# Kernel tuning notes

Hardware: AMD Instinct MI355X
Metric: run time of the kernel (lower is better)

The kernel has to match this reference:

```python
import jax, jax.numpy as jnp
import numpy as np

N_NODES = 100000
N_EDGES = 1600000  # directed, src < dst; to_undirected doubles them
N_GRAPHS = 128
D_IN, D_H, D_FC, N_CLS = 128, 64, 32, 10


def setup_inputs() -> dict:
    key = jax.random.key(0)
    ks = jax.random.split(key, 12)
    x = jax.random.normal(ks[0], (N_NODES, D_IN), dtype=jnp.float32)
    # edges with src < dst so concatenating the flipped copy yields the undirected set
    r = jax.random.randint(ks[1], (2, N_EDGES), 0, N_NODES, dtype=jnp.int64)
    src = jnp.minimum(r[0], r[1])
    dst = jnp.maximum(r[0], r[1])
    dst = jnp.where(src == dst, (dst + 1) % N_NODES, dst)  # avoid pre-existing self loops
    edge_index = jnp.stack([src, dst])
    batch = jnp.sort(jax.random.randint(ks[2], (N_NODES,), 0, N_GRAPHS, dtype=jnp.int64))
    sc = lambda f: 1.0 / jnp.sqrt(jnp.float32(f))
    return {
        "x": x,
        "edge_index": edge_index,
        "batch": batch,
        "W_in": jax.random.normal(ks[3], (D_IN, D_H), jnp.float32) * sc(D_IN),
        "b_in": jnp.zeros((D_H,), jnp.float32),
        "W1": jax.random.normal(ks[4], (D_H, D_H), jnp.float32) * sc(D_H),
        "b1": jnp.zeros((D_H,), jnp.float32),
        "W2": jax.random.normal(ks[5], (D_H, D_H), jnp.float32) * sc(D_H),
        "b2": jnp.zeros((D_H,), jnp.float32),
        "Wf1": jax.random.normal(ks[6], (D_H, D_FC), jnp.float32) * sc(D_H),
        "bf1": jnp.zeros((D_FC,), jnp.float32),
        "Wf2": jax.random.normal(ks[7], (D_FC, N_CLS), jnp.float32) * sc(D_FC),
        "bf2": jnp.zeros((N_CLS,), jnp.float32),
    }


def _gcn_conv(x, W, b, src, dst, dinv, n_nodes):
    # GCNConv: x' = D^{-1/2}(A+I)D^{-1/2} (xW) + b, dinv = deg^{-1/2} incl. self loops
    xw = x @ W
    norm = (dinv[src] * dinv[dst])[:, None]              # [E,1]
    agg = jax.ops.segment_sum(xw[src] * norm, dst, num_segments=n_nodes)
    agg = agg + xw * (dinv * dinv)[:, None]              # self-loop term
    return agg + b


def reference(x, edge_index, batch, W_in, b_in, W1, b1, W2, b2, Wf1, bf1, Wf2, bf2):
    n = x.shape[0]
    # to_undirected: append reversed edges (inputs have src<dst, so no dup dirs)
    src = jnp.concatenate([edge_index[0], edge_index[1]])
    dst = jnp.concatenate([edge_index[1], edge_index[0]])
    # degree including self loop
    deg = 1.0 + jax.ops.segment_sum(jnp.ones_like(dst, dtype=x.dtype), dst, num_segments=n)
    dinv = jax.lax.rsqrt(deg)

    h = jax.nn.relu(x @ W_in + b_in)
    h = jax.nn.relu(_gcn_conv(h, W1, b1, src, dst, dinv, n))
    h = jax.nn.relu(_gcn_conv(h, W2, b2, src, dst, dinv, n))

    # global_mean_pool over graph ids
    sums = jax.ops.segment_sum(h, batch, num_segments=N_GRAPHS)
    cnts = jax.ops.segment_sum(jnp.ones((n,), h.dtype), batch, num_segments=N_GRAPHS)
    pooled = sums / jnp.maximum(cnts, 1.0)[:, None]

    g = jax.nn.relu(pooled @ Wf1 + bf1)
    logits = g @ Wf2 + bf2
    return jax.nn.log_softmax(logits, axis=1)
```

## Files before the change

kernel.cpp:

```cpp
#include <hip/hip_runtime.h>
#include <hip/hip_fp16.h>
#include <math.h>

constexpr int DG  = 128;
constexpr int DIN = 128;
constexpr int DH  = 64;
constexpr int DFC = 32;
constexpr int DC  = 10;
constexpr int CAP    = 80;
constexpr int NB     = 2048;
constexpr int ABLK   = 256;
constexpr int SCAP   = 2048;
constexpr int MAXNPB = 52;

__global__ __launch_bounds__(256) void k_hist(const int* __restrict__ src,
                                              const int* __restrict__ dst,
                                              int* __restrict__ histT,
                                              int E, int EPB, int NPB) {
    __shared__ int h[NB];
    for (int i = threadIdx.x; i < NB; i += 256) h[i] = 0;
    __syncthreads();
    int e0 = blockIdx.x * EPB, e1 = min(e0 + EPB, E);
    for (int i = e0 + threadIdx.x; i < e1; i += 256) {
        int u = src[i], v = dst[i];
        atomicAdd(&h[v / NPB], 1);
        atomicAdd(&h[u / NPB], 1);
    }
    __syncthreads();
    for (int i = threadIdx.x; i < NB; i += 256)
        histT[(size_t)i * ABLK + blockIdx.x] = h[i];
}

__global__ __launch_bounds__(256) void k_expand(const int* __restrict__ histT,
                                                int* __restrict__ baseT,
                                                int* __restrict__ ecnt,
                                                float* __restrict__ sums,
                                                int* __restrict__ cnts) {
    __shared__ int s[256];
    int b = blockIdx.x, t = threadIdx.x;
    int v = histT[(size_t)b * ABLK + t];
    s[t] = v;
    __syncthreads();
    for (int o = 1; o < 256; o <<= 1) {
        int tv = (t >= o) ? s[t - o] : 0;
        __syncthreads();
        s[t] += tv;
        __syncthreads();
    }
    int incl = s[t];
    baseT[(size_t)b * ABLK + t] = b * SCAP + incl - v;
    if (t == 255) ecnt[b] = min(incl, SCAP);
    int gid = b * 256 + t;
    if (gid < DG * DH) sums[gid] = 0.0f;
    if (gid < DG) cnts[gid] = 0;
}

__global__ __launch_bounds__(256) void k_binplace(const int* __restrict__ src,
                                                  const int* __restrict__ dst,
                                                  const int* __restrict__ baseT,
                                                  int* __restrict__ staging,
                                                  int E, int EPB, int NPB) {
    __shared__ int lcnt[NB];
    __shared__ int lbase[NB];
    int blk = blockIdx.x;
    for (int i = threadIdx.x; i < NB; i += 256) {
        lcnt[i]  = 0;
        lbase[i] = baseT[(size_t)i * ABLK + blk];
    }
    __syncthreads();
    int e0 = blk * EPB, e1 = min(e0 + EPB, E);
    for (int i = e0 + threadIdx.x; i < e1; i += 256) {
        int u = src[i], v = dst[i];
        int bv = v / NPB, bu = u / NPB;
        int rv = atomicAdd(&lcnt[bv], 1);
        int sv = lbase[bv] + rv;
        if (sv < (bv + 1) * SCAP) staging[sv] = ((v - bv * NPB) << 17) | u;
        int ru = atomicAdd(&lcnt[bu], 1);
        int su = lbase[bu] + ru;
        if (su < (bu + 1) * SCAP) staging[su] = ((u - bu * NPB) << 17) | v;
    }
}

__global__ __launch_bounds__(256) void k_rows(const int* __restrict__ staging,
                                              const int* __restrict__ ecnt,
                                              int* __restrict__ adj,
                                              int* __restrict__ cnt,
                                              float* __restrict__ dinv,
                                              int N, int NPB) {
    __shared__ int rows[MAXNPB * CAP];
    __shared__ int cur[MAXNPB];
    int b = blockIdx.x;
    int nbase = b * NPB;
    int nn = min(NPB, N - nbase);
    if (nn <= 0) return;
    for (int i = threadIdx.x; i < nn; i += 256) cur[i] = 0;
    __syncthreads();
    int s0 = b * SCAP, s1 = s0 + ecnt[b];
    for (int i = s0 + threadIdx.x; i < s1; i += 256) {
        int e  = staging[i];
        int vl = e >> 17;
        int u  = e & 0x1FFFF;
        int p  = atomicAdd(&cur[vl], 1);
        if (p < CAP) rows[vl * CAP + p] = u;
    }
    __syncthreads();
    for (int s = threadIdx.x; s < nn * CAP; s += 256) {
        int node = s / CAP, p = s - node * CAP;
        if (p < min(cur[node], CAP))
            adj[(size_t)(nbase + node) * CAP + p] = rows[s];
    }
    for (int i = threadIdx.x; i < nn; i += 256) {
        int c = cur[i];
        cnt[nbase + i]  = c;
        dinv[nbase + i] = rsqrtf(1.0f + (float)c);
    }
}

__global__ __launch_bounds__(256) void k_lin_in(const float* __restrict__ x,
                                                const float* __restrict__ W,
                                                const float* __restrict__ b,
                                                __half* __restrict__ out, int n) {
    __shared__ float sx[16 * DIN];
    __shared__ float part[16 * 4 * DH];
    int t = threadIdx.x;
    int lane = t & 63, w = t >> 6;
    float wreg[32];
#pragma unroll
    for (int i = 0; i < 32; i++) wreg[i] = W[(w * 32 + i) * DH + lane];
    float bb = b[lane];
    int tile = blockIdx.x * 16;
    const float4* xsrc = (const float4*)(x + (size_t)tile * DIN);
    float4* sx4 = (float4*)sx;
    sx4[t]       = xsrc[t];
    sx4[t + 256] = xsrc[t + 256];
    __syncthreads();
#pragma unroll 1
    for (int r = 0; r < 16; r++) {
        const float4* xr = (const float4*)(sx + r * DIN + w * 32);
        float a0 = 0.f, a1 = 0.f, a2 = 0.f, a3 = 0.f;
#pragma unroll
        for (int q = 0; q < 8; q++) {
            float4 xv = xr[q];
            a0 = fmaf(xv.x, wreg[q * 4 + 0], a0);
            a1 = fmaf(xv.y, wreg[q * 4 + 1], a1);
            a2 = fmaf(xv.z, wreg[q * 4 + 2], a2);
            a3 = fmaf(xv.w, wreg[q * 4 + 3], a3);
        }
        part[(r * 4 + w) * DH + lane] = (a0 + a1) + (a2 + a3);
    }
    __syncthreads();
#pragma unroll
    for (int q = 0; q < 4; q++) {
        int r = w * 4 + q;
        float s = part[(r * 4 + 0) * DH + lane] + part[(r * 4 + 1) * DH + lane]
                + part[(r * 4 + 2) * DH + lane] + part[(r * 4 + 3) * DH + lane] + bb;
        out[(size_t)(tile + r) * DH + lane] = __float2half(fmaxf(s, 0.0f));
    }
}

__global__ __launch_bounds__(256) void k_mm64(const __half* __restrict__ h,
                                              const float* __restrict__ W,
                                              const float* __restrict__ dinv,
                                              __half* __restrict__ out, int n) {
    __shared__ float sx[16 * DH];
    int t = threadIdx.x, lane = t & 63, w = t >> 6;
    float wreg[64];
#pragma unroll
    for (int i = 0; i < 64; i++) wreg[i] = W[i * DH + lane];
    int tile = blockIdx.x * 16;
    {
        const __half2* hsrc = (const __half2*)(h + (size_t)tile * DH);
        float2* sx2 = (float2*)sx;
        sx2[t * 2]     = __half22float2(hsrc[t * 2]);
        sx2[t * 2 + 1] = __half22float2(hsrc[t * 2 + 1]);
    }
    __syncthreads();
#pragma unroll
    for (int q = 0; q < 4; q++) {
        int r = w * 4 + q;
        const float4* xr = (const float4*)(sx + r * DH);
        float a0 = 0.f, a1 = 0.f, a2 = 0.f, a3 = 0.f;
#pragma unroll
        for (int p = 0; p < 16; p++) {
            float4 xv = xr[p];
            a0 = fmaf(xv.x, wreg[p * 4 + 0], a0);
            a1 = fmaf(xv.y, wreg[p * 4 + 1], a1);
            a2 = fmaf(xv.z, wreg[p * 4 + 2], a2);
            a3 = fmaf(xv.w, wreg[p * 4 + 3], a3);
        }
        float dv = dinv[tile + r];
        out[(size_t)(tile + r) * DH + lane] = __float2half(((a0 + a1) + (a2 + a3)) * dv);
    }
}

__global__ __launch_bounds__(256) void k_gather(const int* __restrict__ cnt,
                                                const int* __restrict__ adj,
                                                const __half2* __restrict__ xws,
                                                const float* __restrict__ dinv,
                                                const float* __restrict__ b,
                                                __half* __restrict__ out, int n) {
    int lane = threadIdx.x & 63;
    int v    = blockIdx.x * 4 + (threadIdx.x >> 6);
    if (v >= n) return;
    int half_id = lane >> 5, fp = lane & 31;
    int len = min(cnt[v], CAP);
    const int* row = adj + (size_t)v * CAP;
    int idx = 0;
    if (lane < len) idx = row[lane];
    int len64 = min(len, 64);
    float ax0 = 0.f, ay0 = 0.f, ax1 = 0.f, ay1 = 0.f;
    float ax2 = 0.f, ay2 = 0.f, ax3 = 0.f, ay3 = 0.f;
    int k = half_id;
    for (; k + 6 < len64; k += 8) {
        int u0 = __shfl(idx, k);
        int u1 = __shfl(idx, k + 2);
        int u2 = __shfl(idx, k + 4);
        int u3 = __shfl(idx, k + 6);
        float2 f0 = __half22float2(xws[(size_t)u0 * 32 + fp]);
        float2 f1 = __half22float2(xws[(size_t)u1 * 32 + fp]);
        float2 f2 = __half22float2(xws[(size_t)u2 * 32 + fp]);
        float2 f3 = __half22float2(xws[(size_t)u3 * 32 + fp]);
        ax0 += f0.x; ay0 += f0.y; ax1 += f1.x; ay1 += f1.y;
        ax2 += f2.x; ay2 += f2.y; ax3 += f3.x; ay3 += f3.y;
    }
    for (; k < len64; k += 2) {
        int u0 = __shfl(idx, k);
        float2 f0 = __half22float2(xws[(size_t)u0 * 32 + fp]);
        ax0 += f0.x; ay0 += f0.y;
    }
    for (int j = 64 + half_id; j < len; j += 2) {
        float2 f0 = __half22float2(xws[(size_t)row[j] * 32 + fp]);
        ax0 += f0.x; ay0 += f0.y;
    }
    float ax = (ax0 + ax1) + (ax2 + ax3);
    float ay = (ay0 + ay1) + (ay2 + ay3);
    ax += __shfl_xor(ax, 32);
    ay += __shfl_xor(ay, 32);
    if (half_id == 0) {
        float2 s  = __half22float2(xws[(size_t)v * 32 + fp]);
        float  dv = dinv[v];
        float2 bb = ((const float2*)b)[fp];
        __half2 o = __floats2half2_rn(fmaxf(dv * (ax + s.x) + bb.x, 0.0f),
                                      fmaxf(dv * (ay + s.y) + bb.y, 0.0f));
        ((__half2*)out)[(size_t)v * 32 + fp] = o;
    }
}

__global__ __launch_bounds__(256) void k_pool(const __half* __restrict__ h,
                                              const int* __restrict__ batch,
                                              float* __restrict__ sums,
                                              int* __restrict__ cnts, int n) {
    int lane = threadIdx.x & 63;
    int w    = blockIdx.x * 4 + (threadIdx.x >> 6);
    int start = w * 64;
    if (start >= n) return;
    int end  = min(start + 64, n);
    int curg = batch[start];
    float acc = 0.f;
    int   c   = 0;
    for (int node = start; node < end; node++) {
        int g = batch[node];
        if (g != curg) {
            atomicAdd(&sums[curg * DH + lane], acc);
            if (lane == 0) atomicAdd(&cnts[curg], c);
            acc = 0.f; c = 0; curg = g;
        }
        acc += __half2float(h[(size_t)node * DH + lane]);
        c++;
    }
    atomicAdd(&sums[curg * DH + lane], acc);
    if (lane == 0) atomicAdd(&cnts[curg], c);
}

__global__ __launch_bounds__(64) void k_head(const float* __restrict__ sums,
                                             const int* __restrict__ cnts,
                                             const float* __restrict__ Wf1,
                                             const float* __restrict__ bf1,
                                             const float* __restrict__ Wf2,
                                             const float* __restrict__ bf2,
                                             float* __restrict__ out) {
    int g = blockIdx.x, lane = threadIdx.x;
    float cnt    = (float)max(cnts[g], 1);
    float pooled = sums[g * DH + lane] / cnt;
    float acc = (lane < DFC) ? bf1[lane] : 0.f;
    for (int k = 0; k < DH; k++) {
        float pk = __shfl(pooled, k);
        if (lane < DFC) acc = fmaf(pk, Wf1[k * DFC + lane], acc);
    }
    float gv = fmaxf(acc, 0.f);
    float acc2 = (lane < DC) ? bf2[lane] : 0.f;
    for (int k = 0; k < DFC; k++) {
        float gk = __shfl(gv, k);
        if (lane < DC) acc2 = fmaf(gk, Wf2[k * DC + lane], acc2);
    }
    float v = (lane < DC) ? acc2 : -INFINITY;
    float m = v;
    for (int o = 8; o; o >>= 1) m = fmaxf(m, __shfl_xor(m, o));
    float e = (lane < DC) ? expf(v - m) : 0.f;
    float s = e;
    for (int o = 8; o; o >>= 1) s += __shfl_xor(s, o);
    if (lane < DC) out[g * DC + lane] = v - m - logf(s);
}

extern "C" void kernel_launch(void* const* d_in, const int* in_sizes, int n_in,
                              void* d_out, int out_size, void* d_ws, size_t ws_size,
                              hipStream_t stream) {
    const float* x    = (const float*)d_in[0];
    const int*   ei   = (const int*)d_in[1];
    const int*   batch= (const int*)d_in[2];
    const float* W_in = (const float*)d_in[3];
    const float* b_in = (const float*)d_in[4];
    const float* W1   = (const float*)d_in[5];
    const float* b1   = (const float*)d_in[6];
    const float* W2   = (const float*)d_in[7];
    const float* b2   = (const float*)d_in[8];
    const float* Wf1  = (const float*)d_in[9];
    const float* bf1  = (const float*)d_in[10];
    const float* Wf2  = (const float*)d_in[11];
    const float* bf2  = (const float*)d_in[12];
    float* out = (float*)d_out;

    const int E = in_sizes[1] / 2;
    const int N = in_sizes[0] / DIN;
    const int* src = ei;
    const int* dst = ei + E;

    const int NPB = (N + NB - 1) / NB;
    const int NBU = (N + NPB - 1) / NPB;
    const int EPB = (E + ABLK - 1) / ABLK;

    char* ws = (char*)d_ws;
    size_t off = 0;
    auto alloc = [&](size_t bytes) -> void* {
        void* p = ws + off;
        off = (off + bytes + 255) & ~(size_t)255;
        return p;
    };
    int*    cnt     = (int*)   alloc((size_t)N * 4);
    float*  dinv    = (float*) alloc((size_t)N * 4);
    int*    adj     = (int*)   alloc((size_t)N * CAP * 4);
    int*    histT   = (int*)   alloc((size_t)ABLK * NB * 4);
    int*    baseT   = (int*)   alloc((size_t)ABLK * NB * 4);
    int*    ecnt    = (int*)   alloc((size_t)NB * 4);
    int*    staging = (int*)   alloc((size_t)NB * SCAP * 4);
    __half* hA      = (__half*)alloc((size_t)N * DH * 2);
    __half* hX      = (__half*)alloc((size_t)N * DH * 2);
    float*  sums    = (float*) alloc((size_t)DG * DH * 4);
    int*    cnts    = (int*)   alloc((size_t)DG * 4);

    k_hist<<<ABLK, 256, 0, stream>>>(src, dst, histT, E, EPB, NPB);
    k_expand<<<NB, 256, 0, stream>>>(histT, baseT, ecnt, sums, cnts);
    k_binplace<<<ABLK, 256, 0, stream>>>(src, dst, baseT, staging, E, EPB, NPB);
    k_rows<<<NBU, 256, 0, stream>>>(staging, ecnt, adj, cnt, dinv, N, NPB);

    k_lin_in<<<N / 16, 256, 0, stream>>>(x, W_in, b_in, hA, N);

    k_mm64<<<N / 16, 256, 0, stream>>>(hA, W1, dinv, hX, N);
    k_gather<<<(N + 3) / 4, 256, 0, stream>>>(cnt, adj, (const __half2*)hX, dinv, b1, hA, N);

    k_mm64<<<N / 16, 256, 0, stream>>>(hA, W2, dinv, hX, N);
    k_gather<<<(N + 3) / 4, 256, 0, stream>>>(cnt, adj, (const __half2*)hX, dinv, b2, hA, N);

    int pw = (N + 63) / 64;
    k_pool<<<(pw + 3) / 4, 256, 0, stream>>>(hA, batch, sums, cnts, N);

    k_head<<<DG, 64, 0, stream>>>(sums, cnts, Wf1, bf1, Wf2, bf2, out);
}
```

Measured before the change: 319.3 us.

## Fuse input linear with first GCN matmul and pair half2 adds in gather

The input projection kernel now also applies W1 and the dinv scaling, keeping the ReLU'd hidden tile in shared memory. This removes one kernel launch and a full fp16 write and read of the hidden activations. The gather loop is unrolled to 8 neighbours per iteration, sums pairs in half precision before converting to float, and uses shift/or byte addressing. Pairwise fp16 adds lose some precision, and the larger unroll and the extra 64-element weight array raise register pressure.

Result: no change. 318.5 us (-0.2%).

```diff
diff --git a/kernel.cpp b/kernel.cpp
--- a/kernel.cpp
+++ b/kernel.cpp
@@ -116,18 +116,21 @@
     }
 }
 
-__global__ __launch_bounds__(256) void k_lin_in(const float* __restrict__ x,
-                                                const float* __restrict__ W,
-                                                const float* __restrict__ b,
-                                                __half* __restrict__ out, int n) {
+__global__ __launch_bounds__(256) void k_lin2(const float* __restrict__ x,
+                                              const float* __restrict__ Wi,
+                                              const float* __restrict__ bi,
+                                              const float* __restrict__ W1,
+                                              const float* __restrict__ dinv,
+                                              __half* __restrict__ out, int n) {
     __shared__ float sx[16 * DIN];
     __shared__ float part[16 * 4 * DH];
+    __shared__ float sh[16 * DH];
     int t = threadIdx.x;
     int lane = t & 63, w = t >> 6;
     float wreg[32];
 #pragma unroll
-    for (int i = 0; i < 32; i++) wreg[i] = W[(w * 32 + i) * DH + lane];
-    float bb = b[lane];
+    for (int i = 0; i < 32; i++) wreg[i] = Wi[(w * 32 + i) * DH + lane];
+    float bb = bi[lane];
     int tile = blockIdx.x * 16;
     const float4* xsrc = (const float4*)(x + (size_t)tile * DIN);
     float4* sx4 = (float4*)sx;
@@ -154,7 +157,27 @@
         int r = w * 4 + q;
         float s = part[(r * 4 + 0) * DH + lane] + part[(r * 4 + 1) * DH + lane]
                 + part[(r * 4 + 2) * DH + lane] + part[(r * 4 + 3) * DH + lane] + bb;
-        out[(size_t)(tile + r) * DH + lane] = __float2half(fmaxf(s, 0.0f));
+        sh[r * DH + lane] = fmaxf(s, 0.0f);
+    }
+    float w1[64];
+#pragma unroll
+    for (int i = 0; i < 64; i++) w1[i] = W1[i * DH + lane];
+    __syncthreads();
+#pragma unroll
+    for (int q = 0; q < 4; q++) {
+        int r = w * 4 + q;
+        const float4* hr = (const float4*)(sh + r * DH);
+        float a0 = 0.f, a1 = 0.f, a2 = 0.f, a3 = 0.f;
+#pragma unroll
+        for (int p = 0; p < 16; p++) {
+            float4 xv = hr[p];
+            a0 = fmaf(xv.x, w1[p * 4 + 0], a0);
+            a1 = fmaf(xv.y, w1[p * 4 + 1], a1);
+            a2 = fmaf(xv.z, w1[p * 4 + 2], a2);
+            a3 = fmaf(xv.w, w1[p * 4 + 3], a3);
+        }
+        float dv = dinv[tile + r];
+        out[(size_t)(tile + r) * DH + lane] = __float2half(((a0 + a1) + (a2 + a3)) * dv);
     }
 }
 
@@ -208,32 +231,43 @@
     int idx = 0;
     if (lane < len) idx = row[lane];
     int len64 = min(len, 64);
-    float ax0 = 0.f, ay0 = 0.f, ax1 = 0.f, ay1 = 0.f;
-    float ax2 = 0.f, ay2 = 0.f, ax3 = 0.f, ay3 = 0.f;
+    const char* xb = (const char*)xws;
+    int fpo = fp << 2;
+    float ax = 0.f, ay = 0.f;
     int k = half_id;
-    for (; k + 6 < len64; k += 8) {
+    for (; k + 14 < len64; k += 16) {
         int u0 = __shfl(idx, k);
         int u1 = __shfl(idx, k + 2);
         int u2 = __shfl(idx, k + 4);
         int u3 = __shfl(idx, k + 6);
-        float2 f0 = __half22float2(xws[(size_t)u0 * 32 + fp]);
-        float2 f1 = __half22float2(xws[(size_t)u1 * 32 + fp]);
-        float2 f2 = __half22float2(xws[(size_t)u2 * 32 + fp]);
-        float2 f3 = __half22float2(xws[(size_t)u3 * 32 + fp]);
-        ax0 += f0.x; ay0 += f0.y; ax1 += f1.x; ay1 += f1.y;
-        ax2 += f2.x; ay2 += f2.y; ax3 += f3.x; ay3 += f3.y;
+        int u4 = __shfl(idx, k + 8);
+        int u5 = __shfl(idx, k + 10);
+        int u6 = __shfl(idx, k + 12);
+        int u7 = __shfl(idx, k + 14);
+        __half2 h0 = *(const __half2*)(xb + ((u0 << 7) | fpo));
+        __half2 h1 = *(const __half2*)(xb + ((u1 << 7) | fpo));
+        __half2 h2 = *(const __half2*)(xb + ((u2 << 7) | fpo));
+        __half2 h3 = *(const __half2*)(xb + ((u3 << 7) | fpo));
+        h0 = __hadd2(h0, *(const __half2*)(xb + ((u4 << 7) | fpo)));
+        h1 = __hadd2(h1, *(const __half2*)(xb + ((u5 << 7) | fpo)));
+        h2 = __hadd2(h2, *(const __half2*)(xb + ((u6 << 7) | fpo)));
+        h3 = __hadd2(h3, *(const __half2*)(xb + ((u7 << 7) | fpo)));
+        float2 f0 = __half22float2(h0);
+        float2 f1 = __half22float2(h1);
+        float2 f2 = __half22float2(h2);
+        float2 f3 = __half22float2(h3);
+        ax += (f0.x + f1.x) + (f2.x + f3.x);
+        ay += (f0.y + f1.y) + (f2.y + f3.y);
     }
     for (; k < len64; k += 2) {
         int u0 = __shfl(idx, k);
-        float2 f0 = __half22float2(xws[(size_t)u0 * 32 + fp]);
-        ax0 += f0.x; ay0 += f0.y;
+        float2 f0 = __half22float2(*(const __half2*)(xb + ((u0 << 7) | fpo)));
+        ax += f0.x; ay += f0.y;
     }
     for (int j = 64 + half_id; j < len; j += 2) {
         float2 f0 = __half22float2(xws[(size_t)row[j] * 32 + fp]);
-        ax0 += f0.x; ay0 += f0.y;
-    }
-    float ax = (ax0 + ax1) + (ax2 + ax3);
-    float ay = (ay0 + ay1) + (ay2 + ay3);
+        ax += f0.x; ay += f0.y;
+    }
     ax += __shfl_xor(ax, 32);
     ay += __shfl_xor(ay, 32);
     if (half_id == 0) {
@@ -353,9 +387,8 @@
     k_binplace<<<ABLK, 256, 0, stream>>>(src, dst, baseT, staging, E, EPB, NPB);
     k_rows<<<NBU, 256, 0, stream>>>(staging, ecnt, adj, cnt, dinv, N, NPB);
 
-    k_lin_in<<<N / 16, 256, 0, stream>>>(x, W_in, b_in, hA, N);
-
-    k_mm64<<<N / 16, 256, 0, stream>>>(hA, W1, dinv, hX, N);
+    k_lin2<<<N / 16, 256, 0, stream>>>(x, W_in, b_in, W1, dinv, hX, N);
+
     k_gather<<<(N + 3) / 4, 256, 0, stream>>>(cnt, adj, (const __half2*)hX, dinv, b1, hA, N);
 
     k_mm64<<<N / 16, 256, 0, stream>>>(hA, W2, dinv, hX, N);
```
